# Kernel optimization log

Measured on AMD Instinct MI355X. Metric: run time of the kernel, lower is better.

The kernel has to match this reference:

```python
import jax, jax.numpy as jnp
import numpy as np

B, D_IN, T = 16, 1024, 4096
CB_SIZE, CB_DIM = 1024, 8
EPS = 1e-12  # F.normalize eps


def _wn_weight(v, g):
    # weight_norm over dim=0: per-output-row normalization. v: [out, in], g: [out]
    return g[:, None] * v / jnp.linalg.norm(v, axis=1, keepdims=True)


def setup_inputs() -> dict:
    key = jax.random.key(0)
    ks = jax.random.split(key, 8)
    z = jax.random.normal(ks[0], (B, D_IN, T), dtype=jnp.float32)
    in_v = jax.random.normal(ks[1], (CB_DIM, D_IN), dtype=jnp.float32) * 0.02
    in_g = jnp.linalg.norm(in_v, axis=1)  # weight_norm init: g = ||v||
    in_b = jnp.zeros((CB_DIM,), dtype=jnp.float32)
    out_v = jax.random.normal(ks[2], (D_IN, CB_DIM), dtype=jnp.float32) * 0.02
    out_g = jnp.linalg.norm(out_v, axis=1)
    out_b = jnp.zeros((D_IN,), dtype=jnp.float32)
    codebook = jax.random.normal(ks[3], (CB_SIZE, CB_DIM), dtype=jnp.float32)
    return {"z": z, "in_v": in_v, "in_g": in_g, "in_b": in_b,
            "out_v": out_v, "out_g": out_g, "out_b": out_b, "codebook": codebook}


def reference(z, in_v, in_g, in_b, out_v, out_g, out_b, codebook):
    # in_proj: 1x1 weight-normed conv, z: [B, D_IN, T] -> z_e: [B, CB_DIM, T]
    w_in = _wn_weight(in_v, in_g)
    z_e = jnp.einsum('od,bdt->bot', w_in, z) + in_b[None, :, None]

    # decode_latents: (b t) d tokens, L2-normalize, cosine distance, argmin
    enc = z_e.transpose(0, 2, 1).reshape(-1, CB_DIM)              # [(B*T), CB_DIM]
    enc_n = enc / jnp.maximum(jnp.linalg.norm(enc, axis=1, keepdims=True), EPS)
    cb_n = codebook / jnp.maximum(jnp.linalg.norm(codebook, axis=1, keepdims=True), EPS)
    dist = (jnp.sum(enc_n ** 2, axis=1, keepdims=True)
            - 2.0 * enc_n @ cb_n.T
            + jnp.sum(cb_n ** 2, axis=1)[None, :])                # [(B*T), CB_SIZE]
    indices = jnp.argmax(-dist, axis=1).reshape(B, T)             # argmin of dist
    z_q = codebook[indices].transpose(0, 2, 1)                    # [B, CB_DIM, T]

    commitment_loss = jnp.mean((z_e - jax.lax.stop_gradient(z_q)) ** 2, axis=(1, 2))
    codebook_loss = jnp.mean((z_q - jax.lax.stop_gradient(z_e)) ** 2, axis=(1, 2))

    # straight-through estimator
    z_q_st = z_e + jax.lax.stop_gradient(z_q - z_e)

    # out_proj: 1x1 weight-normed conv back to input_dim
    w_out = _wn_weight(out_v, out_g)
    z_out = jnp.einsum('od,bdt->bot', w_out, z_q_st) + out_b[None, :, None]
    return (z_out, commitment_loss, codebook_loss, indices, z_e)
```

## Files before the change

### kernel.cpp

```cpp
#include <hip/hip_runtime.h>
#include <math.h>


namespace {
constexpr int kB  = 16;
constexpr int kD  = 1024;
constexpr int kT  = 4096;
constexpr int kCB = 1024;
constexpr int kC  = 8;
constexpr float kEps = 1e-12f;

constexpr size_t N_ZOUT    = (size_t)kB * kD * kT;
constexpr size_t OFF_COMMIT = N_ZOUT;
constexpr size_t OFF_CBL    = OFF_COMMIT + kB;
constexpr size_t OFF_IDX    = OFF_CBL + kB;
constexpr size_t OFF_ZE     = OFF_IDX + (size_t)kB * kT;
}

__global__ void vq_prep(const float* __restrict__ in_v, const float* __restrict__ in_g,
                        const float* __restrict__ out_v, const float* __restrict__ out_g,
                        const float* __restrict__ cb,
                        float* __restrict__ w_in_t, float* __restrict__ w_out_t,
                        float* __restrict__ cb_n_t)
{
    __shared__ float red[4];
    const int blk = blockIdx.x;
    const int tid = threadIdx.x;
    if (blk < 8) {
        const int o = blk;
        float ss = 0.f;
        for (int d = tid; d < kD; d += 256) {
            float v = in_v[o * kD + d];
            ss = fmaf(v, v, ss);
        }
        #pragma unroll
        for (int off = 32; off; off >>= 1) ss += __shfl_xor(ss, off);
        if ((tid & 63) == 0) red[tid >> 6] = ss;
        __syncthreads();
        const float scale = in_g[o] / sqrtf(red[0] + red[1] + red[2] + red[3]);
        for (int d = tid; d < kD; d += 256)
            w_in_t[d * kC + o] = scale * in_v[o * kD + d];
    } else if (blk < 12) {
        const int r = (blk - 8) * 256 + tid;
        float4 a = reinterpret_cast<const float4*>(cb)[2 * r];
        float4 b = reinterpret_cast<const float4*>(cb)[2 * r + 1];
        float n = sqrtf(a.x*a.x + a.y*a.y + a.z*a.z + a.w*a.w +
                        b.x*b.x + b.y*b.y + b.z*b.z + b.w*b.w);
        float s = 1.f / fmaxf(n, kEps);
        a.x *= s; a.y *= s; a.z *= s; a.w *= s;
        b.x *= s; b.y *= s; b.z *= s; b.w *= s;
        reinterpret_cast<float4*>(cb_n_t)[2 * r]     = a;
        reinterpret_cast<float4*>(cb_n_t)[2 * r + 1] = b;
    } else {
        const int r = (blk - 12) * 256 + tid;
        float4 a = reinterpret_cast<const float4*>(out_v)[2 * r];
        float4 b = reinterpret_cast<const float4*>(out_v)[2 * r + 1];
        float n = sqrtf(a.x*a.x + a.y*a.y + a.z*a.z + a.w*a.w +
                        b.x*b.x + b.y*b.y + b.z*b.z + b.w*b.w);
        float s = out_g[r] / n;
        a.x *= s; a.y *= s; a.z *= s; a.w *= s;
        b.x *= s; b.y *= s; b.z *= s; b.w *= s;
        reinterpret_cast<float4*>(w_out_t)[2 * r]     = a;
        reinterpret_cast<float4*>(w_out_t)[2 * r + 1] = b;
    }
}

__global__ __launch_bounds__(256)
void vq_encode(const float* __restrict__ z,
               const float* __restrict__ in_b,
               const float* __restrict__ cb,
               const float* __restrict__ w_in_t,
               const float* __restrict__ cb_n_t,
               float* __restrict__ zq_ws,
               float* __restrict__ out)
{
    __shared__ float s_red[4][kC][64];
    __shared__ float s_ze[kC][64];
    __shared__ float s_sim[16][64];
    __shared__ int   s_idx[16][64];

    const int tid = threadIdx.x;
    const int tg = tid & 15;
    const int sl = tid >> 4;
    const int wv = tid >> 6;
    const int g0 = blockIdx.x * 64;
    const int b  = g0 >> 12;
    const int t0 = g0 & (kT - 1);

    const float* zp = z + ((size_t)b * kD + (size_t)sl * 64) * kT + t0 + 4 * tg;
    const float4* wq = reinterpret_cast<const float4*>(w_in_t) + (size_t)sl * 128;
    float acc[kC][4];
    #pragma unroll
    for (int c = 0; c < kC; c++)
        #pragma unroll
        for (int j = 0; j < 4; j++) acc[c][j] = 0.f;

    #pragma unroll 4
    for (int i = 0; i < 64; i++) {
        const float4 zv = *reinterpret_cast<const float4*>(zp + (size_t)i * kT);
        const float4 w0 = wq[2 * i];
        const float4 w1 = wq[2 * i + 1];
        const float zl[4] = {zv.x, zv.y, zv.z, zv.w};
        const float wl[kC] = {w0.x, w0.y, w0.z, w0.w, w1.x, w1.y, w1.z, w1.w};
        #pragma unroll
        for (int c = 0; c < kC; c++)
            #pragma unroll
            for (int j = 0; j < 4; j++)
                acc[c][j] = fmaf(zl[j], wl[c], acc[c][j]);
    }
    #pragma unroll
    for (int c = 0; c < kC; c++)
        #pragma unroll
        for (int j = 0; j < 4; j++) {
            float v = acc[c][j];
            v += __shfl_xor(v, 16);
            v += __shfl_xor(v, 32);
            acc[c][j] = v;
        }
    if ((tid & 48) == 0) {
        #pragma unroll
        for (int c = 0; c < kC; c++)
            #pragma unroll
            for (int j = 0; j < 4; j++) s_red[wv][c][4 * tg + j] = acc[c][j];
    }
    __syncthreads();

    {
        const int c  = tid >> 5;
        const int t2 = (tid & 31) * 2;
        #pragma unroll
        for (int k = 0; k < 2; k++) {
            const int t = t2 + k;
            s_ze[c][t] = s_red[0][c][t] + s_red[1][c][t] + s_red[2][c][t]
                       + s_red[3][c][t] + in_b[c];
        }
    }
    __syncthreads();

    float zef[4][kC];
    #pragma unroll
    for (int j = 0; j < 4; j++)
        #pragma unroll
        for (int c = 0; c < kC; c++) zef[j][c] = s_ze[c][4 * tg + j];

    float best[4] = {-INFINITY, -INFINITY, -INFINITY, -INFINITY};
    int   bk[4]   = {sl * 64, sl * 64, sl * 64, sl * 64};
    const float4* cq = reinterpret_cast<const float4*>(cb_n_t) + (size_t)sl * 128;
    #pragma unroll 2
    for (int i = 0; i < 64; i++) {
        const float4 c0 = cq[2 * i];
        const float4 c1 = cq[2 * i + 1];
        const float cl[kC] = {c0.x, c0.y, c0.z, c0.w, c1.x, c1.y, c1.z, c1.w};
        #pragma unroll
        for (int j = 0; j < 4; j++) {
            float sim = zef[j][0] * cl[0];
            #pragma unroll
            for (int c = 1; c < kC; c++) sim = fmaf(zef[j][c], cl[c], sim);
            if (sim > best[j]) { best[j] = sim; bk[j] = sl * 64 + i; }
        }
    }
    #pragma unroll
    for (int j = 0; j < 4; j++) {
        s_sim[sl][4 * tg + j] = best[j];
        s_idx[sl][4 * tg + j] = bk[j];
    }
    __syncthreads();

    if (tid < 64) {
        const int t = tid;
        float bs = s_sim[0][t];
        int   bi = s_idx[0][t];
        #pragma unroll
        for (int g = 1; g < 16; g++) {
            const float v = s_sim[g][t];
            if (v > bs) { bs = v; bi = s_idx[g][t]; }
        }
        out[OFF_IDX + (size_t)b * kT + t0 + t] = (float)bi;

        const float4 q0 = reinterpret_cast<const float4*>(cb)[2 * bi];
        const float4 q1 = reinterpret_cast<const float4*>(cb)[2 * bi + 1];
        const float zq[kC] = {q0.x, q0.y, q0.z, q0.w, q1.x, q1.y, q1.z, q1.w};

        float lsum = 0.f;
        #pragma unroll
        for (int c = 0; c < kC; c++) {
            const float ze = s_ze[c][t];
            const float d = ze - zq[c];
            lsum = fmaf(d, d, lsum);
            out[OFF_ZE + (size_t)b * (kC * kT) + (size_t)c * kT + t0 + t] = ze;
            zq_ws[((size_t)b * kC + c) * kT + t0 + t] = zq[c];
        }
        #pragma unroll
        for (int off = 32; off; off >>= 1) lsum += __shfl_xor(lsum, off);
        if (tid == 0) {
            const float lv = lsum * (1.f / (kC * kT));
            atomicAdd(&out[OFF_COMMIT + b], lv);
            atomicAdd(&out[OFF_CBL + b], lv);
        }
    }
}

__global__ __launch_bounds__(256)
void vq_out(const float* __restrict__ zq_ws,
            const float* __restrict__ w_out_t, const float* __restrict__ out_b,
            float* __restrict__ out)
{
    const int tid = threadIdx.x;
    for (int row = blockIdx.x; row < kB * kD; row += gridDim.x) {
        const int b = row >> 10;
        const int o = row & (kD - 1);
        const float4 w0 = reinterpret_cast<const float4*>(w_out_t)[2 * o];
        const float4 w1 = reinterpret_cast<const float4*>(w_out_t)[2 * o + 1];
        const float wl[kC] = {w0.x, w0.y, w0.z, w0.w, w1.x, w1.y, w1.z, w1.w};
        const float bias = out_b[o];
        const float4* zqp = reinterpret_cast<const float4*>(zq_ws)
                          + (size_t)b * kC * (kT / 4);
        float4* op = reinterpret_cast<float4*>(out) + (size_t)row * (kT / 4);
        #pragma unroll
        for (int k = 0; k < 4; k++) {
            const int t4 = k * 256 + tid;
            float q[kC][4];
            #pragma unroll
            for (int c = 0; c < kC; c++) {
                const float4 qv = zqp[c * (kT / 4) + t4];
                q[c][0] = qv.x; q[c][1] = qv.y; q[c][2] = qv.z; q[c][3] = qv.w;
            }
            float rr[4];
            #pragma unroll
            for (int j = 0; j < 4; j++) {
                float v = bias;
                #pragma unroll
                for (int c = 0; c < kC; c++) v = fmaf(q[c][j], wl[c], v);
                rr[j] = v;
            }
            op[t4] = make_float4(rr[0], rr[1], rr[2], rr[3]);
        }
    }
}

extern "C" void kernel_launch(void* const* d_in, const int* in_sizes, int n_in,
                              void* d_out, int out_size, void* d_ws, size_t ws_size,
                              hipStream_t stream) {
    const float* z     = (const float*)d_in[0];
    const float* in_v  = (const float*)d_in[1];
    const float* in_g  = (const float*)d_in[2];
    const float* in_b  = (const float*)d_in[3];
    const float* out_v = (const float*)d_in[4];
    const float* out_g = (const float*)d_in[5];
    const float* out_b = (const float*)d_in[6];
    const float* cb    = (const float*)d_in[7];
    float* out = (float*)d_out;

    float* w_in_t  = (float*)d_ws;
    float* w_out_t = w_in_t + (size_t)kD * kC;
    float* cb_n_t  = w_out_t + (size_t)kD * kC;
    float* zq_ws   = cb_n_t + (size_t)kCB * kC;

    vq_prep<<<16, 256, 0, stream>>>(in_v, in_g, out_v, out_g, cb,
                                    w_in_t, w_out_t, cb_n_t);
    (void)hipMemsetAsync(out + OFF_COMMIT, 0, 2 * kB * sizeof(float), stream);
    vq_encode<<<(kB * kT) / 64, 256, 0, stream>>>(z, in_b, cb, w_in_t, cb_n_t,
                                                  zq_ws, out);
    vq_out<<<2048, 256, 0, stream>>>(zq_ws, w_out_t, out_b, out);
}
```

Baseline: 526.5 us.

## Widen encode blocks to 512 threads and tile out-proj for zq register reuse

The encode kernel now runs 512 threads per block, so each of 32 slices reduces over 32 input channels and searches 32 codebook entries, with the cross-slice reductions widened to match. The out-projection kernel is retiled: each block loads one 1024-wide time chunk of z_q into registers once and reuses it across 64 output rows, with weights and biases staged in shared memory. This removes the repeated z_q reloads per output row and raises parallelism in the memory-bound encode phase. In exchange it uses more shared memory and adds a longer final argmax reduction over 32 partials.

Measured after the change: 520.5 us. Within noise of the previous version (-1.2%).

```diff
diff --git a/kernel.cpp b/kernel.cpp
--- a/kernel.cpp
+++ b/kernel.cpp
@@ -65,7 +65,7 @@
     }
 }
 
-__global__ __launch_bounds__(256)
+__global__ __launch_bounds__(512)
 void vq_encode(const float* __restrict__ z,
                const float* __restrict__ in_b,
                const float* __restrict__ cb,
@@ -74,10 +74,10 @@
                float* __restrict__ zq_ws,
                float* __restrict__ out)
 {
-    __shared__ float s_red[4][kC][64];
+    __shared__ float s_red[8][kC][64];
     __shared__ float s_ze[kC][64];
-    __shared__ float s_sim[16][64];
-    __shared__ int   s_idx[16][64];
+    __shared__ float s_sim[32][64];
+    __shared__ int   s_idx[32][64];
 
     const int tid = threadIdx.x;
     const int tg = tid & 15;
@@ -87,16 +87,16 @@
     const int b  = g0 >> 12;
     const int t0 = g0 & (kT - 1);
 
-    const float* zp = z + ((size_t)b * kD + (size_t)sl * 64) * kT + t0 + 4 * tg;
-    const float4* wq = reinterpret_cast<const float4*>(w_in_t) + (size_t)sl * 128;
+    const float* zp = z + ((size_t)b * kD + (size_t)sl * 32) * kT + t0 + 4 * tg;
+    const float4* wq = reinterpret_cast<const float4*>(w_in_t) + (size_t)sl * 64;
     float acc[kC][4];
     #pragma unroll
     for (int c = 0; c < kC; c++)
         #pragma unroll
         for (int j = 0; j < 4; j++) acc[c][j] = 0.f;
 
-    #pragma unroll 4
-    for (int i = 0; i < 64; i++) {
+    #pragma unroll 8
+    for (int i = 0; i < 32; i++) {
         const float4 zv = *reinterpret_cast<const float4*>(zp + (size_t)i * kT);
         const float4 w0 = wq[2 * i];
         const float4 w1 = wq[2 * i + 1];
@@ -126,14 +126,12 @@
     __syncthreads();
 
     {
-        const int c  = tid >> 5;
-        const int t2 = (tid & 31) * 2;
-        #pragma unroll
-        for (int k = 0; k < 2; k++) {
-            const int t = t2 + k;
-            s_ze[c][t] = s_red[0][c][t] + s_red[1][c][t] + s_red[2][c][t]
-                       + s_red[3][c][t] + in_b[c];
-        }
+        const int c = tid >> 6;
+        const int t = tid & 63;
+        float v = in_b[c];
+        #pragma unroll
+        for (int w = 0; w < 8; w++) v += s_red[w][c][t];
+        s_ze[c][t] = v;
     }
     __syncthreads();
 
@@ -144,10 +142,10 @@
         for (int c = 0; c < kC; c++) zef[j][c] = s_ze[c][4 * tg + j];
 
     float best[4] = {-INFINITY, -INFINITY, -INFINITY, -INFINITY};
-    int   bk[4]   = {sl * 64, sl * 64, sl * 64, sl * 64};
-    const float4* cq = reinterpret_cast<const float4*>(cb_n_t) + (size_t)sl * 128;
-    #pragma unroll 2
-    for (int i = 0; i < 64; i++) {
+    int   bk[4]   = {sl * 32, sl * 32, sl * 32, sl * 32};
+    const float4* cq = reinterpret_cast<const float4*>(cb_n_t) + (size_t)sl * 64;
+    #pragma unroll 4
+    for (int i = 0; i < 32; i++) {
         const float4 c0 = cq[2 * i];
         const float4 c1 = cq[2 * i + 1];
         const float cl[kC] = {c0.x, c0.y, c0.z, c0.w, c1.x, c1.y, c1.z, c1.w};
@@ -156,7 +154,7 @@
             float sim = zef[j][0] * cl[0];
             #pragma unroll
             for (int c = 1; c < kC; c++) sim = fmaf(zef[j][c], cl[c], sim);
-            if (sim > best[j]) { best[j] = sim; bk[j] = sl * 64 + i; }
+            if (sim > best[j]) { best[j] = sim; bk[j] = sl * 32 + i; }
         }
     }
     #pragma unroll
@@ -171,7 +169,7 @@
         float bs = s_sim[0][t];
         int   bi = s_idx[0][t];
         #pragma unroll
-        for (int g = 1; g < 16; g++) {
+        for (int g = 1; g < 32; g++) {
             const float v = s_sim[g][t];
             if (v > bs) { bs = v; bi = s_idx[g][t]; }
         }
@@ -205,36 +203,51 @@
             const float* __restrict__ w_out_t, const float* __restrict__ out_b,
             float* __restrict__ out)
 {
+    __shared__ float s_w[64][kC + 1];
+    __shared__ float s_bias[64];
+
     const int tid = threadIdx.x;
-    for (int row = blockIdx.x; row < kB * kD; row += gridDim.x) {
-        const int b = row >> 10;
-        const int o = row & (kD - 1);
+    const int blk = blockIdx.x;
+    const int b   = blk >> 6;
+    const int tc  = (blk >> 4) & 3;
+    const int og  = blk & 15;
+
+    if (tid < 64) {
+        const int o = og * 64 + tid;
         const float4 w0 = reinterpret_cast<const float4*>(w_out_t)[2 * o];
         const float4 w1 = reinterpret_cast<const float4*>(w_out_t)[2 * o + 1];
-        const float wl[kC] = {w0.x, w0.y, w0.z, w0.w, w1.x, w1.y, w1.z, w1.w};
-        const float bias = out_b[o];
-        const float4* zqp = reinterpret_cast<const float4*>(zq_ws)
-                          + (size_t)b * kC * (kT / 4);
-        float4* op = reinterpret_cast<float4*>(out) + (size_t)row * (kT / 4);
-        #pragma unroll
-        for (int k = 0; k < 4; k++) {
-            const int t4 = k * 256 + tid;
-            float q[kC][4];
-            #pragma unroll
-            for (int c = 0; c < kC; c++) {
-                const float4 qv = zqp[c * (kT / 4) + t4];
-                q[c][0] = qv.x; q[c][1] = qv.y; q[c][2] = qv.z; q[c][3] = qv.w;
-            }
-            float rr[4];
-            #pragma unroll
-            for (int j = 0; j < 4; j++) {
-                float v = bias;
-                #pragma unroll
-                for (int c = 0; c < kC; c++) v = fmaf(q[c][j], wl[c], v);
-                rr[j] = v;
-            }
-            op[t4] = make_float4(rr[0], rr[1], rr[2], rr[3]);
-        }
+        s_w[tid][0] = w0.x; s_w[tid][1] = w0.y; s_w[tid][2] = w0.z; s_w[tid][3] = w0.w;
+        s_w[tid][4] = w1.x; s_w[tid][5] = w1.y; s_w[tid][6] = w1.z; s_w[tid][7] = w1.w;
+        s_bias[tid] = out_b[o];
+    }
+
+    const float4* zqp = reinterpret_cast<const float4*>(zq_ws)
+                      + (size_t)b * kC * (kT / 4) + tc * 256 + tid;
+    float q[kC][4];
+    #pragma unroll
+    for (int c = 0; c < kC; c++) {
+        const float4 qv = zqp[c * (kT / 4)];
+        q[c][0] = qv.x; q[c][1] = qv.y; q[c][2] = qv.z; q[c][3] = qv.w;
+    }
+    __syncthreads();
+
+    float* op = out + ((size_t)b * kD + (size_t)og * 64) * kT + tc * 1024 + 4 * tid;
+    #pragma unroll 4
+    for (int i = 0; i < 64; i++) {
+        float wl[kC];
+        #pragma unroll
+        for (int c = 0; c < kC; c++) wl[c] = s_w[i][c];
+        const float bias = s_bias[i];
+        float rr[4];
+        #pragma unroll
+        for (int j = 0; j < 4; j++) {
+            float v = bias;
+            #pragma unroll
+            for (int c = 0; c < kC; c++) v = fmaf(q[c][j], wl[c], v);
+            rr[j] = v;
+        }
+        *reinterpret_cast<float4*>(op + (size_t)i * kT) =
+            make_float4(rr[0], rr[1], rr[2], rr[3]);
     }
 }
 
@@ -259,7 +272,7 @@
     vq_prep<<<16, 256, 0, stream>>>(in_v, in_g, out_v, out_g, cb,
                                     w_in_t, w_out_t, cb_n_t);
     (void)hipMemsetAsync(out + OFF_COMMIT, 0, 2 * kB * sizeof(float), stream);
-    vq_encode<<<(kB * kT) / 64, 256, 0, stream>>>(z, in_b, cb, w_in_t, cb_n_t,
+    vq_encode<<<(kB * kT) / 64, 512, 0, stream>>>(z, in_b, cb, w_in_t, cb_n_t,
                                                   zq_ws, out);
-    vq_out<<<2048, 256, 0, stream>>>(zq_ws, w_out_t, out_b, out);
-}
+    vq_out<<<1024, 256, 0, stream>>>(zq_ws, w_out_t, out_b, out);
+}
```
